# Kernel optimization log

Hardware: AMD Instinct MI355X
Metric: run time of the kernel (lower is better)

## Reference

```python
import jax, jax.numpy as jnp
import numpy as np

B = 32768
IN_DIM, OUT_DIM, VAR_DIM = 2, 3, 50
KER_DIMS = [1024, 1024, 1024, 1024]
NSTEPS = 32  # fixed-step RK4 stand-in for adaptive odeint over t in [0, 1]


def setup_inputs() -> dict:
    key = jax.random.key(0)
    ks = jax.random.split(key, 11)
    x = jax.random.normal(ks[0], (B, IN_DIM), dtype=jnp.float32)
    dims = [VAR_DIM] + KER_DIMS + [VAR_DIM]
    inp = {"x": x}
    for i, (d1, d2) in enumerate(zip(dims[:-1], dims[1:])):
        # torch Linear(d1+1, d2): weight (d2, d1+1); stored here as (d1+1, d2)
        bound = 1.0 / np.sqrt(d1 + 1)
        inp[f"W{i}"] = jax.random.uniform(ks[1 + 2 * i], (d1 + 1, d2), jnp.float32, -bound, bound)
        inp[f"b{i}"] = jax.random.uniform(ks[2 + 2 * i], (d2,), jnp.float32, -bound, bound)
    return inp


def _odefunc(t, y, Ws, bs):
    # Each layer: concat time column, Linear, ReLU (except last) -- matches ODEfunc.forward
    out = y
    n = len(Ws)
    for i in range(n):
        tcol = jnp.full((out.shape[0], 1), t, dtype=out.dtype)
        h = jnp.concatenate([out, tcol], axis=1)
        out = h @ Ws[i] + bs[i]
        if i < n - 1:
            out = jax.nn.relu(out)
    return out


def _integrate(x, Ws, bs):
    # Pad input into var_dim state: out[:, :in_dim] = x, rest zeros
    y0 = jnp.zeros((x.shape[0], VAR_DIM), dtype=x.dtype).at[:, : x.shape[1]].set(x)
    dt = jnp.asarray(1.0 / NSTEPS, dtype=x.dtype)
    ts = jnp.arange(NSTEPS, dtype=x.dtype) * dt

    def step(y, t):
        k1 = _odefunc(t, y, Ws, bs)
        k2 = _odefunc(t + dt * 0.5, y + dt * 0.5 * k1, Ws, bs)
        k3 = _odefunc(t + dt * 0.5, y + dt * 0.5 * k2, Ws, bs)
        k4 = _odefunc(t + dt, y + dt * k3, Ws, bs)
        return y + (dt / 6.0) * (k1 + 2.0 * k2 + 2.0 * k3 + k4), None

    y1, _ = jax.lax.scan(step, y0, ts)
    return y1[:, :OUT_DIM]


def reference(x, W0, b0, W1, b1, W2, b2, W3, b3, W4, b4):
    Ws = (W0, W1, W2, W3, W4)
    bs = (b0, b1, b2, b3, b4)
    return _integrate(x, Ws, bs)
```

## Files before the change

### kernel.cpp

```cpp
#include <hip/hip_runtime.h>
#include <hip/hip_bf16.h>
#include <stdint.h>


typedef __bf16 bf16_t;
typedef bf16_t bf16x8 __attribute__((ext_vector_type(8)));
typedef float  f32x4  __attribute__((ext_vector_type(4)));

#define DEVI static __device__ __forceinline__

DEVI void gload_lds16(const bf16_t* gsrc, bf16_t* ldst) {
  __builtin_amdgcn_global_load_lds(
      (const __attribute__((address_space(1))) uint32_t*)gsrc,
      (__attribute__((address_space(3))) uint32_t*)ldst,
      16, 0, 0);
}

template<int K>
__global__ __launch_bounds__(512, 2) void gemm256(
    const bf16_t* __restrict__ A,
    const bf16_t* __restrict__ BT,
    const float* __restrict__ bias,
    const float* __restrict__ wtime,
    float t,
    bf16_t* __restrict__ C, int ldc,
    int M, int N)
{
  constexpr int NT = K / 64;
  static_assert(NT >= 2, "need >=2 K-tiles");

  __shared__ __align__(16) bf16_t As[2][256][64];
  __shared__ __align__(16) bf16_t Bs[2][256][64];

  const int tid  = threadIdx.x;
  const int wave = tid >> 6;
  const int lane = tid & 63;
  const int wr = wave >> 2;
  const int wc = wave & 3;

  int wg = blockIdx.x;
  {
    const int cpx = gridDim.x >> 3;
    wg = (wg & 7) * cpx + (wg >> 3);
  }
  const int nbn = N >> 8;
  const int bm = (wg / nbn) << 8;
  const int bn = (wg % nbn) << 8;

  const int srow = lane >> 3;
  const int scol = ((lane & 7) << 3) ^ ((lane & 32) >> 1) ^ ((wave & 1) << 5);
  const bf16_t* aS = A  + (size_t)(bm + wave * 8 + srow) * K + scol;
  const bf16_t* bS = BT + (size_t)(bn + wave * 8 + srow) * K + scol;
  bf16_t* aD = &As[0][0][0] + wave * 8 * 64;
  bf16_t* bD = &Bs[0][0][0] + wave * 8 * 64;

  auto stageHalf = [&](int kt, int isB, int h) {
    const int buf = kt & 1;
    const bf16_t* src = (isB ? bS : aS) + (size_t)(h * 128) * K + kt * 64;
    bf16_t*       dst = (isB ? bD : aD) + (buf * 256 + h * 128) * 64;
    gload_lds16(src,                  dst);
    gload_lds16(src + (size_t)64 * K, dst + 64 * 64);
  };
  auto stageTile = [&](int kt) {
    stageHalf(kt, 0, 0); stageHalf(kt, 0, 1);
    stageHalf(kt, 1, 0); stageHalf(kt, 1, 1);
  };

  const int fr = lane & 15;
  const int fq = lane >> 4;
  const int rsw = ((fr & 4) << 3) ^ ((fr & 8) << 3);

  bf16x8 ah0[8], ah1[8];
  bf16x8 bh0[4], bh1[4];
  f32x4  acc[8][4] = {};

  auto lda_into = [&](bf16x8 (&dst)[8], int buf, int mh) {
    const char* base = (const char*)&As[buf][0][0];
#pragma unroll
    for (int m = 0; m < 4; ++m)
#pragma unroll
      for (int kk = 0; kk < 2; ++kk) {
        int r  = wr * 128 + (mh * 4 + m) * 16 + fr;
        int cb = (kk * 64 + fq * 16) ^ rsw;
        dst[m * 2 + kk] = *(const bf16x8*)(base + r * 128 + cb);
      }
  };
  auto ldb_into = [&](bf16x8 (&dst)[4], int buf, int nh) {
    const char* base = (const char*)&Bs[buf][0][0];
#pragma unroll
    for (int n = 0; n < 2; ++n)
#pragma unroll
      for (int kk = 0; kk < 2; ++kk) {
        int r  = wc * 64 + (nh * 2 + n) * 16 + fr;
        int cb = (kk * 64 + fq * 16) ^ rsw;
        dst[n * 2 + kk] = *(const bf16x8*)(base + r * 128 + cb);
      }
  };
  auto mma_quad = [&](bf16x8 (&a)[8], bf16x8 (&b)[4], int mh, int nh) {
    __builtin_amdgcn_s_setprio(1);
#pragma unroll
    for (int m = 0; m < 4; ++m)
#pragma unroll
      for (int n = 0; n < 2; ++n)
#pragma unroll
        for (int kk = 0; kk < 2; ++kk)
          acc[mh * 4 + m][nh * 2 + n] = __builtin_amdgcn_mfma_f32_16x16x32_bf16(
              a[m * 2 + kk], b[n * 2 + kk],
              acc[mh * 4 + m][nh * 2 + n], 0, 0, 0);
    __builtin_amdgcn_s_setprio(0);
  };

  stageTile(0);
  asm volatile("s_waitcnt vmcnt(0)" ::: "memory");
  __builtin_amdgcn_s_barrier();
  lda_into(ah0, 0, 0);
  ldb_into(bh0, 0, 0);

  for (int t2 = 0; t2 < NT; ++t2) {
    const int buf = t2 & 1;
    if (t2 + 1 < NT) stageTile(t2 + 1);
    ldb_into(bh1, buf, 1);
    mma_quad(ah0, bh0, 0, 0);
    lda_into(ah1, buf, 1);
    mma_quad(ah0, bh1, 0, 1);
    mma_quad(ah1, bh0, 1, 0);
    if (t2 + 1 < NT) {
      asm volatile("s_waitcnt vmcnt(0)" ::: "memory");
      __builtin_amdgcn_s_barrier();
      lda_into(ah0, buf ^ 1, 0);
      ldb_into(bh0, buf ^ 1, 0);
    }
    mma_quad(ah1, bh1, 1, 1);
  }

#pragma unroll
  for (int n = 0; n < 4; ++n) {
    const int gcol = bn + wc * 64 + n * 16 + fr;
    const float bv = bias[gcol] + t * wtime[gcol];
#pragma unroll
    for (int m = 0; m < 8; ++m) {
      const int grow0 = bm + wr * 128 + m * 16 + (fq << 2);
#pragma unroll
      for (int r = 0; r < 4; ++r) {
        float v = acc[m][n][r] + bv;
        v = v > 0.0f ? v : 0.0f;
        C[(size_t)(grow0 + r) * ldc + gcol] = (bf16_t)v;
      }
    }
  }
}

template<int BM, int BN, int BK, int WROWS, int WCOLS, bool RELU, bool OUT_BF16>
__global__ __launch_bounds__(256) void gemm_bt(
    const bf16_t* __restrict__ A, int lda,
    const bf16_t* __restrict__ BT,
    const float* __restrict__ bias,
    const float* __restrict__ wtime,
    float t,
    void* __restrict__ Cv, int ldc,
    int M, int K)
{
  static_assert(BK == 64, "swizzle assumes BK=64");
  constexpr int MR  = BM / WROWS / 16;
  constexpr int NR  = BN / WCOLS / 16;
  constexpr int TPR = BK / 8;
  constexpr int RPW = 64 / TPR;
  constexpr int RPL = 4 * RPW;
  static_assert(BM % RPL == 0 && BN % RPL == 0, "tile staging mismatch");

  __shared__ bf16_t As[BM][BK];
  __shared__ bf16_t Bs[BN][BK];

  const int tid  = threadIdx.x;
  const int wave = tid >> 6;
  const int lane = tid & 63;
  const int wr = wave / WCOLS;
  const int wc = wave % WCOLS;
  const int bm = blockIdx.x * BM;
  const int bn = blockIdx.y * BN;
  const int lrow = lane >> 3;
  const int lcol = (((lane & 7) << 3) ^ ((lane & 32) >> 1) ^ ((wave & 1) << 5));

  const int fr = lane & 15;
  const int fq = lane >> 4;
  const int esw = ((fr & 4) << 2) ^ ((fr & 8) << 2);

  f32x4 acc[MR][NR] = {};

  for (int k0 = 0; k0 < K; k0 += BK) {
#pragma unroll
    for (int i = 0; i < BM / RPL; ++i) {
      const int rb = i * RPL + wave * RPW;
      gload_lds16(&A[(size_t)(bm + rb + lrow) * lda + k0 + lcol], &As[rb][0]);
    }
#pragma unroll
    for (int i = 0; i < BN / RPL; ++i) {
      const int rb = i * RPL + wave * RPW;
      gload_lds16(&BT[(size_t)(bn + rb + lrow) * K + k0 + lcol], &Bs[rb][0]);
    }
    __syncthreads();
#pragma unroll
    for (int kk = 0; kk < BK / 32; ++kk) {
      bf16x8 af[MR], bfr[NR];
      const int ecol = (kk * 32 + fq * 8) ^ esw;
#pragma unroll
      for (int m = 0; m < MR; ++m)
        af[m] = *(const bf16x8*)&As[wr * (BM / WROWS) + m * 16 + fr][ecol];
#pragma unroll
      for (int n = 0; n < NR; ++n)
        bfr[n] = *(const bf16x8*)&Bs[wc * (BN / WCOLS) + n * 16 + fr][ecol];
#pragma unroll
      for (int m = 0; m < MR; ++m)
#pragma unroll
        for (int n = 0; n < NR; ++n)
          acc[m][n] = __builtin_amdgcn_mfma_f32_16x16x32_bf16(
              af[m], bfr[n], acc[m][n], 0, 0, 0);
    }
    __syncthreads();
  }

#pragma unroll
  for (int n = 0; n < NR; ++n) {
    const int gcol = bn + wc * (BN / WCOLS) + n * 16 + fr;
    const float bv = bias[gcol] + t * wtime[gcol];
#pragma unroll
    for (int m = 0; m < MR; ++m) {
      const int grow0 = bm + wr * (BM / WROWS) + m * 16 + (fq << 2);
#pragma unroll
      for (int r = 0; r < 4; ++r) {
        float v = acc[m][n][r] + bv;
        if (RELU) v = v > 0.0f ? v : 0.0f;
        if constexpr (OUT_BF16)
          ((bf16_t*)Cv)[(size_t)(grow0 + r) * ldc + gcol] = (bf16_t)v;
        else
          ((float*)Cv)[(size_t)(grow0 + r) * ldc + gcol] = v;
      }
    }
  }
}

__global__ __launch_bounds__(256) void gemm_l4_rk4_l0(
    const bf16_t* __restrict__ A, int lda,
    const bf16_t* __restrict__ BT,
    const float* __restrict__ bias,
    const float* __restrict__ wtime,
    float t,
    const bf16_t* __restrict__ BT0,
    const float* __restrict__ bias0,
    const float* __restrict__ wtime0,
    float tn,
    float* __restrict__ y, float* __restrict__ accb,
    bf16_t* __restrict__ act0,
    float ca, float cs, int mode,
    int M, int K)
{
  constexpr int BM = 64, BN = 64, BK = 64;
  constexpr int MR = 2, NR = 2;

  __shared__ bf16_t As[BM][BK];
  __shared__ bf16_t Bs[BN][BK];
  __shared__ bf16_t Ys[64][72];

  const int tid  = threadIdx.x;
  const int wave = tid >> 6;
  const int lane = tid & 63;
  const int wr = wave >> 1;
  const int wc = wave & 1;
  const int bm = blockIdx.x * BM;
  const int lrow = lane >> 3;
  const int lcol = (((lane & 7) << 3) ^ ((lane & 32) >> 1) ^ ((wave & 1) << 5));

  const int fr = lane & 15;
  const int fq = lane >> 4;
  const int esw = ((fr & 4) << 2) ^ ((fr & 8) << 2);

  f32x4 acc[MR][NR] = {};

  for (int k0 = 0; k0 < K; k0 += BK) {
#pragma unroll
    for (int i = 0; i < 2; ++i) {
      const int rb = i * 32 + wave * 8;
      gload_lds16(&A[(size_t)(bm + rb + lrow) * lda + k0 + lcol], &As[rb][0]);
    }
#pragma unroll
    for (int i = 0; i < 2; ++i) {
      const int rb = i * 32 + wave * 8;
      gload_lds16(&BT[(size_t)(rb + lrow) * K + k0 + lcol], &Bs[rb][0]);
    }
    __syncthreads();
#pragma unroll
    for (int kk = 0; kk < 2; ++kk) {
      bf16x8 af[MR], bfr[NR];
      const int ecol = (kk * 32 + fq * 8) ^ esw;
#pragma unroll
      for (int m = 0; m < MR; ++m)
        af[m] = *(const bf16x8*)&As[wr * 32 + m * 16 + fr][ecol];
#pragma unroll
      for (int n = 0; n < NR; ++n)
        bfr[n] = *(const bf16x8*)&Bs[wc * 32 + n * 16 + fr][ecol];
#pragma unroll
      for (int m = 0; m < MR; ++m)
#pragma unroll
        for (int n = 0; n < NR; ++n)
          acc[m][n] = __builtin_amdgcn_mfma_f32_16x16x32_bf16(
              af[m], bfr[n], acc[m][n], 0, 0, 0);
    }
    __syncthreads();
  }

#pragma unroll
  for (int n = 0; n < NR; ++n) {
    const int gcol = wc * 32 + n * 16 + fr;
    const float bv = bias[gcol] + t * wtime[gcol];
#pragma unroll
    for (int m = 0; m < MR; ++m) {
      const int lr0 = wr * 32 + m * 16 + (fq << 2);
#pragma unroll
      for (int r = 0; r < 4; ++r) {
        const float kv = acc[m][n][r] + bv;
        const size_t o = (size_t)(bm + lr0 + r) * 64 + gcol;
        float yb;
        if (mode == 0) {
          accb[o] = kv;
          yb = y[o] + cs * kv;
        } else if (mode == 1) {
          accb[o] += ca * kv;
          yb = y[o] + cs * kv;
        } else {
          const float ny = y[o] + cs * (accb[o] + kv);
          y[o] = ny;
          yb = ny;
        }
        Ys[lr0 + r][gcol] = (bf16_t)yb;
      }
    }
  }
  __syncthreads();

  const int colbase = wave * 256;
  bf16x8 af0[4][2];
#pragma unroll
  for (int m2 = 0; m2 < 4; ++m2)
#pragma unroll
    for (int kk = 0; kk < 2; ++kk)
      af0[m2][kk] = *(const bf16x8*)&Ys[m2 * 16 + fr][kk * 32 + fq * 8];

  bf16x8 bfA[4][2], bfB[4][2];
  auto ldb0 = [&](bf16x8 (&d)[4][2], int g) {
#pragma unroll
    for (int n = 0; n < 4; ++n)
#pragma unroll
      for (int kk = 0; kk < 2; ++kk)
        d[n][kk] = *(const bf16x8*)(BT0
            + (size_t)(colbase + g * 64 + n * 16 + fr) * 64 + kk * 32 + fq * 8);
  };
  ldb0(bfA, 0);

#pragma unroll
  for (int g = 0; g < 4; ++g) {
    bf16x8 (&bcur)[4][2]  = (g & 1) ? bfB : bfA;
    bf16x8 (&bnext)[4][2] = (g & 1) ? bfA : bfB;
    if (g + 1 < 4) ldb0(bnext, g + 1);
    f32x4 acc2[4][4] = {};
#pragma unroll
    for (int kk = 0; kk < 2; ++kk)
#pragma unroll
      for (int m2 = 0; m2 < 4; ++m2)
#pragma unroll
        for (int n = 0; n < 4; ++n)
          acc2[m2][n] = __builtin_amdgcn_mfma_f32_16x16x32_bf16(
              af0[m2][kk], bcur[n][kk], acc2[m2][n], 0, 0, 0);
#pragma unroll
    for (int n = 0; n < 4; ++n) {
      const int col = colbase + g * 64 + n * 16 + fr;
      const float bv = bias0[col] + tn * wtime0[col];
#pragma unroll
      for (int m2 = 0; m2 < 4; ++m2) {
        const int row0 = bm + m2 * 16 + (fq << 2);
#pragma unroll
        for (int r = 0; r < 4; ++r) {
          float v = acc2[m2][n][r] + bv;
          v = v > 0.0f ? v : 0.0f;
          act0[(size_t)(row0 + r) * 1024 + col] = (bf16_t)v;
        }
      }
    }
  }
}

__global__ void prep_weight(const float* __restrict__ W, const float* __restrict__ b,
                            bf16_t* __restrict__ WT, float* __restrict__ bias,
                            float* __restrict__ wtime,
                            int K, int N, int Kpad, int Npad)
{
  int idx = blockIdx.x * 256 + threadIdx.x;
  int total = Npad * Kpad;
  if (idx < total) {
    int n = idx / Kpad, k = idx % Kpad;
    float v = (n < N && k < K) ? W[(size_t)k * N + n] : 0.0f;
    WT[idx] = (bf16_t)v;
  }
  if (idx < Npad) {
    bias[idx]  = (idx < N) ? b[idx] : 0.0f;
    wtime[idx] = (idx < N) ? W[(size_t)K * N + idx] : 0.0f;
  }
}

__global__ void init_y(const float* __restrict__ x, float* __restrict__ y,
                       bf16_t* __restrict__ ybf, int M)
{
  int i = blockIdx.x * 256 + threadIdx.x;
  if (i < M * 64) {
    int m = i >> 6, c = i & 63;
    float v = (c < 2) ? x[m * 2 + c] : 0.0f;
    y[i] = v;
    ybf[i] = (bf16_t)v;
  }
}

__global__ void extract_out(const float* __restrict__ y, float* __restrict__ out, int M)
{
  int i = blockIdx.x * 256 + threadIdx.x;
  if (i < M * 3) {
    int m = i / 3, c = i % 3;
    out[i] = y[(size_t)m * 64 + c];
  }
}

extern "C" void kernel_launch(void* const* d_in, const int* in_sizes, int n_in,
                              void* d_out, int out_size, void* d_ws, size_t ws_size,
                              hipStream_t stream)
{
  (void)in_sizes; (void)n_in; (void)out_size; (void)ws_size;
  const int M = 32768;

  const float* x = (const float*)d_in[0];
  const float* Wp[5]; const float* bp[5];
  for (int i = 0; i < 5; ++i) {
    Wp[i] = (const float*)d_in[1 + 2 * i];
    bp[i] = (const float*)d_in[2 + 2 * i];
  }

  char* ws = (char*)d_ws; size_t off = 0;
  auto alloc = [&](size_t bytes) -> char* {
    char* p = ws + off; off += (bytes + 255) & ~(size_t)255; return p;
  };

  bf16_t* WT[5];
  WT[0] = (bf16_t*)alloc((size_t)1024 * 64 * 2);
  WT[1] = (bf16_t*)alloc((size_t)1024 * 1024 * 2);
  WT[2] = (bf16_t*)alloc((size_t)1024 * 1024 * 2);
  WT[3] = (bf16_t*)alloc((size_t)1024 * 1024 * 2);
  WT[4] = (bf16_t*)alloc((size_t)64 * 1024 * 2);
  float* bias[5]; float* wtm[5];
  for (int i = 0; i < 5; ++i) {
    int Np = (i == 4) ? 64 : 1024;
    bias[i] = (float*)alloc((size_t)Np * 4);
    wtm[i]  = (float*)alloc((size_t)Np * 4);
  }
  float*  y    = (float*)alloc((size_t)M * 64 * 4);
  float*  accb = (float*)alloc((size_t)M * 64 * 4);
  bf16_t* ybf  = (bf16_t*)alloc((size_t)M * 64 * 2);
  bf16_t* act0 = (bf16_t*)alloc((size_t)M * 1024 * 2);
  bf16_t* act1 = (bf16_t*)alloc((size_t)M * 1024 * 2);

  const int Kd[5]  = {50, 1024, 1024, 1024, 1024};
  const int Nd[5]  = {1024, 1024, 1024, 1024, 50};
  const int Kpd[5] = {64, 1024, 1024, 1024, 1024};
  const int Npd[5] = {1024, 1024, 1024, 1024, 64};
  for (int i = 0; i < 5; ++i) {
    int tot = Npd[i] * Kpd[i];
    prep_weight<<<dim3((tot + 255) / 256), 256, 0, stream>>>(
        Wp[i], bp[i], WT[i], bias[i], wtm[i], Kd[i], Nd[i], Kpd[i], Npd[i]);
  }

  init_y<<<dim3((M * 64 + 255) / 256), 256, 0, stream>>>(x, y, ybf, M);

  const float dtv = 1.0f / 32.0f;
  dim3 gL0(M / 128, 1024 / 128);
  dim3 g256(M / 256 * (1024 / 256));
  dim3 gL4(M / 64);

  gemm_bt<128,128,64,2,2,true,true><<<gL0, 256, 0, stream>>>(
      ybf, 64, WT[0], bias[0], wtm[0], 0.0f, act0, 1024, M, 64);

  auto run_eval = [&](float t, float tn, float ca, float cs, int mode) {
    gemm256<1024><<<g256, 512, 0, stream>>>(
        act0, WT[1], bias[1], wtm[1], t, act1, 1024, M, 1024);
    gemm256<1024><<<g256, 512, 0, stream>>>(
        act1, WT[2], bias[2], wtm[2], t, act0, 1024, M, 1024);
    gemm256<1024><<<g256, 512, 0, stream>>>(
        act0, WT[3], bias[3], wtm[3], t, act1, 1024, M, 1024);
    gemm_l4_rk4_l0<<<gL4, 256, 0, stream>>>(
        act1, 1024, WT[4], bias[4], wtm[4], t,
        WT[0], bias[0], wtm[0], tn,
        y, accb, act0, ca, cs, mode, M, 1024);
  };

  for (int i = 0; i < 32; ++i) {
    const float t0 = i * dtv;
    const float tm = t0 + 0.5f * dtv;
    const float t1 = t0 + dtv;
    const float t0n = (i + 1) * dtv;
    run_eval(t0, tm,  0.0f, 0.5f * dtv, 0);
    run_eval(tm, tm,  2.0f, 0.5f * dtv, 1);
    run_eval(tm, t1,  2.0f, dtv,        1);
    run_eval(t1, t0n, 0.0f, dtv / 6.0f, 2);
  }

  extract_out<<<dim3((M * 3 + 255) / 256), 256, 0, stream>>>(y, (float*)d_out, M);
}
```

Baseline: 33.69 ms.

## Double-buffer LDS tiles in fused last-layer GEMM to overlap loads with MFMA

Changes the K loop of the fused layer-4/RK4/layer-0 kernel to use two LDS buffers for A and B. The next tile is prefetched with global_load_lds while the current tile's MFMAs run, and fragment loads are split into two kk halves that are software-pipelined. This is meant to hide global memory latency and halve the barriers per iteration, at the cost of doubling LDS use for the tiles, which may reduce occupancy.

Result: no change. 33.63 ms (-0.2%).

```diff
diff --git a/kernel.cpp b/kernel.cpp
--- a/kernel.cpp
+++ b/kernel.cpp
@@ -254,11 +254,11 @@
     float ca, float cs, int mode,
     int M, int K)
 {
-  constexpr int BM = 64, BN = 64, BK = 64;
   constexpr int MR = 2, NR = 2;
-
-  __shared__ bf16_t As[BM][BK];
-  __shared__ bf16_t Bs[BN][BK];
+  const int NT = K / 64;
+
+  __shared__ __align__(16) bf16_t As[2][64][64];
+  __shared__ __align__(16) bf16_t Bs[2][64][64];
   __shared__ bf16_t Ys[64][72];
 
   const int tid  = threadIdx.x;
@@ -266,46 +266,70 @@
   const int lane = tid & 63;
   const int wr = wave >> 1;
   const int wc = wave & 1;
-  const int bm = blockIdx.x * BM;
+  const int bm = blockIdx.x * 64;
   const int lrow = lane >> 3;
   const int lcol = (((lane & 7) << 3) ^ ((lane & 32) >> 1) ^ ((wave & 1) << 5));
+
+  const bf16_t* aS = A  + (size_t)(bm + wave * 8 + lrow) * lda + lcol;
+  const bf16_t* bS = BT + (size_t)(wave * 8 + lrow) * K + lcol;
+  bf16_t* aD = &As[0][0][0] + wave * 8 * 64;
+  bf16_t* bD = &Bs[0][0][0] + wave * 8 * 64;
+
+  auto stage = [&](int kt) {
+    const int buf = kt & 1;
+    gload_lds16(aS + kt * 64,                      aD + buf * 64 * 64);
+    gload_lds16(aS + (size_t)32 * lda + kt * 64,   aD + buf * 64 * 64 + 32 * 64);
+    gload_lds16(bS + kt * 64,                      bD + buf * 64 * 64);
+    gload_lds16(bS + (size_t)32 * K + kt * 64,     bD + buf * 64 * 64 + 32 * 64);
+  };
 
   const int fr = lane & 15;
   const int fq = lane >> 4;
   const int esw = ((fr & 4) << 2) ^ ((fr & 8) << 2);
 
+  bf16x8 af0[2], af1[2], bf0[2], bf1[2];
   f32x4 acc[MR][NR] = {};
 
-  for (int k0 = 0; k0 < K; k0 += BK) {
-#pragma unroll
-    for (int i = 0; i < 2; ++i) {
-      const int rb = i * 32 + wave * 8;
-      gload_lds16(&A[(size_t)(bm + rb + lrow) * lda + k0 + lcol], &As[rb][0]);
-    }
-#pragma unroll
-    for (int i = 0; i < 2; ++i) {
-      const int rb = i * 32 + wave * 8;
-      gload_lds16(&BT[(size_t)(rb + lrow) * K + k0 + lcol], &Bs[rb][0]);
-    }
-    __syncthreads();
-#pragma unroll
-    for (int kk = 0; kk < 2; ++kk) {
-      bf16x8 af[MR], bfr[NR];
-      const int ecol = (kk * 32 + fq * 8) ^ esw;
-#pragma unroll
-      for (int m = 0; m < MR; ++m)
-        af[m] = *(const bf16x8*)&As[wr * 32 + m * 16 + fr][ecol];
-#pragma unroll
-      for (int n = 0; n < NR; ++n)
-        bfr[n] = *(const bf16x8*)&Bs[wc * 32 + n * 16 + fr][ecol];
-#pragma unroll
-      for (int m = 0; m < MR; ++m)
-#pragma unroll
-        for (int n = 0; n < NR; ++n)
-          acc[m][n] = __builtin_amdgcn_mfma_f32_16x16x32_bf16(
-              af[m], bfr[n], acc[m][n], 0, 0, 0);
-    }
-    __syncthreads();
+  auto ldaf = [&](bf16x8 (&d)[2], int buf, int kk) {
+    const int ecol = (kk * 32 + fq * 8) ^ esw;
+#pragma unroll
+    for (int m = 0; m < 2; ++m)
+      d[m] = *(const bf16x8*)&As[buf][wr * 32 + m * 16 + fr][ecol];
+  };
+  auto ldbf = [&](bf16x8 (&d)[2], int buf, int kk) {
+    const int ecol = (kk * 32 + fq * 8) ^ esw;
+#pragma unroll
+    for (int n = 0; n < 2; ++n)
+      d[n] = *(const bf16x8*)&Bs[buf][wc * 32 + n * 16 + fr][ecol];
+  };
+  auto mma = [&](bf16x8 (&a)[2], bf16x8 (&b)[2]) {
+#pragma unroll
+    for (int m = 0; m < 2; ++m)
+#pragma unroll
+      for (int n = 0; n < 2; ++n)
+        acc[m][n] = __builtin_amdgcn_mfma_f32_16x16x32_bf16(
+            a[m], b[n], acc[m][n], 0, 0, 0);
+  };
+
+  stage(0);
+  asm volatile("s_waitcnt vmcnt(0)" ::: "memory");
+  __builtin_amdgcn_s_barrier();
+  ldaf(af0, 0, 0);
+  ldbf(bf0, 0, 0);
+
+  for (int t2 = 0; t2 < NT; ++t2) {
+    const int buf = t2 & 1;
+    if (t2 + 1 < NT) stage(t2 + 1);
+    ldaf(af1, buf, 1);
+    ldbf(bf1, buf, 1);
+    mma(af0, bf0);
+    if (t2 + 1 < NT) {
+      asm volatile("s_waitcnt vmcnt(0)" ::: "memory");
+      __builtin_amdgcn_s_barrier();
+      ldaf(af0, buf ^ 1, 0);
+      ldbf(bf0, buf ^ 1, 0);
+    }
+    mma(af1, bf1);
   }
 
 #pragma unroll
@@ -338,12 +362,12 @@
   __syncthreads();
 
   const int colbase = wave * 256;
-  bf16x8 af0[4][2];
+  bf16x8 af0v[4][2];
 #pragma unroll
   for (int m2 = 0; m2 < 4; ++m2)
 #pragma unroll
     for (int kk = 0; kk < 2; ++kk)
-      af0[m2][kk] = *(const bf16x8*)&Ys[m2 * 16 + fr][kk * 32 + fq * 8];
+      af0v[m2][kk] = *(const bf16x8*)&Ys[m2 * 16 + fr][kk * 32 + fq * 8];
 
   bf16x8 bfA[4][2], bfB[4][2];
   auto ldb0 = [&](bf16x8 (&d)[4][2], int g) {
@@ -369,7 +393,7 @@
 #pragma unroll
         for (int n = 0; n < 4; ++n)
           acc2[m2][n] = __builtin_amdgcn_mfma_f32_16x16x32_bf16(
-              af0[m2][kk], bcur[n][kk], acc2[m2][n], 0, 0, 0);
+              af0v[m2][kk], bcur[n][kk], acc2[m2][n], 0, 0, 0);
 #pragma unroll
     for (int n = 0; n < 4; ++n) {
       const int col = colbase + g * 64 + n * 16 + fr;
```
